# Kernel tuning notes

Measured on AMD Instinct MI355X. Metric: run time of the kernel, lower is better.

Reference implementation:

```python
import jax, jax.numpy as jnp
import numpy as np

N_NODES = 50000
N_EDGES = 400000
N_GRAPHS = 64
D_IN = 200
D_HID = 32
N_CLASS = 2


def setup_inputs() -> dict:
    key = jax.random.key(0)
    ks = jax.random.split(key, 16)
    x = jax.random.normal(ks[0], (N_NODES, D_IN), dtype=jnp.float32)
    edge_index = jax.random.randint(ks[1], (2, N_EDGES), 0, N_NODES, dtype=jnp.int64)
    edge_attr = jax.random.normal(ks[2], (N_EDGES,), dtype=jnp.float32)
    batch = jnp.sort(jax.random.randint(ks[3], (N_NODES,), 0, N_GRAPHS, dtype=jnp.int64))
    s = 0.05
    params = dict(
        W1r=jax.random.normal(ks[4], (D_IN, D_HID), jnp.float32) * s,
        W1l=jax.random.normal(ks[5], (D_IN, D_HID), jnp.float32) * s,
        b1=jnp.zeros((D_HID,), jnp.float32),
        W2r=jax.random.normal(ks[6], (D_HID, D_HID), jnp.float32) * s,
        W2l=jax.random.normal(ks[7], (D_HID, D_HID), jnp.float32) * s,
        b2=jnp.zeros((D_HID,), jnp.float32),
        W3r=jax.random.normal(ks[8], (D_HID, D_HID), jnp.float32) * s,
        W3l=jax.random.normal(ks[9], (D_HID, D_HID), jnp.float32) * s,
        b3=jnp.zeros((D_HID,), jnp.float32),
        Wlin=jax.random.normal(ks[10], (D_HID, N_CLASS), jnp.float32) * s,
        blin=jnp.zeros((N_CLASS,), jnp.float32),
    )
    return dict(x=x, edge_index=edge_index, edge_attr=edge_attr, batch=batch, **params)


def _graph_conv(x, src, dst, Wr, Wl, b):
    # PyG GraphConv: out_i = lin_rel(sum_{j->i} x_j) + lin_root(x_i)
    agg = jax.ops.segment_sum(x[src], dst, num_segments=x.shape[0])  # [N, d_in]
    return agg @ Wr + b + x @ Wl


def reference(x, edge_index, edge_attr, batch,
              W1r, W1l, b1, W2r, W2l, b2, W3r, W3l, b3, Wlin, blin):
    src, dst = edge_index[0], edge_index[1]
    # dropout is identity at inference (training=False)
    h = jax.nn.elu(_graph_conv(x, src, dst, W1r, W1l, b1))
    h = jax.nn.elu(_graph_conv(h, src, dst, W2r, W2l, b2))
    h = jax.nn.elu(_graph_conv(h, src, dst, W3r, W3l, b3))
    # global mean pool over graphs
    sums = jax.ops.segment_sum(h, batch, num_segments=N_GRAPHS)  # [G, d]
    counts = jax.ops.segment_sum(jnp.ones((h.shape[0],), h.dtype), batch,
                                 num_segments=N_GRAPHS)
    pooled = sums / jnp.maximum(counts, 1.0)[:, None]
    logits = pooled @ Wlin + blin
    return jax.nn.log_softmax(logits, axis=1)
```

## Files before the change

### kernel.cpp

```cpp
#include <hip/hip_runtime.h>
#include <hip/hip_bf16.h>


#define D_IN 200
#define N_GRAPHS 64

#define KP 232
#define KB 7
#define WT_ELEMS (64 * KP)
#define W23_ELEMS 2048

#define NT 256
#define NSCB 196
#define HS_STR 40

typedef __attribute__((ext_vector_type(8))) short bf16x8;
typedef __attribute__((ext_vector_type(4))) float f32x4;

__device__ __forceinline__ float4 elu4(float4 v) {
    float4 o;
    o.x = (v.x > 0.f) ? v.x : expm1f(v.x);
    o.y = (v.y > 0.f) ? v.y : expm1f(v.y);
    o.z = (v.z > 0.f) ? v.z : expm1f(v.z);
    o.w = (v.w > 0.f) ? v.w : expm1f(v.w);
    return o;
}

__global__ __launch_bounds__(NT) void count_pack(const int* __restrict__ dst,
                                                 int* __restrict__ cnt,
                                                 int* __restrict__ rank, int E,
                                                 const float* __restrict__ W1r,
                                                 const float* __restrict__ W1l,
                                                 const float* __restrict__ W2r,
                                                 const float* __restrict__ W2l,
                                                 const float* __restrict__ W3r,
                                                 const float* __restrict__ W3l,
                                                 __hip_bfloat16* __restrict__ Wt,
                                                 __hip_bfloat16* __restrict__ Wt2,
                                                 __hip_bfloat16* __restrict__ Wt3,
                                                 int egrid, int wgrid) {
    int blk = blockIdx.x;
    if (blk < egrid) {
        int e = blk * NT + threadIdx.x;
        if (e < E) rank[e] = atomicAdd(&cnt[dst[e]], 1);
    } else if (blk < egrid + wgrid) {
        int idx = (blk - egrid) * NT + threadIdx.x;
        if (idx < WT_ELEMS) {
            int n = idx / KP, k = idx % KP;
            float v = 0.f;
            if (k < D_IN) v = (n < 32) ? W1r[k * 32 + n] : W1l[k * 32 + (n - 32)];
            Wt[idx] = __float2bfloat16(v);
        }
    } else {
        int idx = (blk - egrid - wgrid) * NT + threadIdx.x;
        if (idx < 2 * W23_ELEMS) {
            int which = idx >> 11;
            int j = idx & 2047;
            int n = j >> 5, k = j & 31;
            const float* Wr = which ? W3r : W2r;
            const float* Wl = which ? W3l : W2l;
            float v = (n < 32) ? Wr[k * 32 + n] : Wl[k * 32 + (n - 32)];
            (which ? Wt3 : Wt2)[j] = __float2bfloat16(v);
        }
    }
}

__global__ __launch_bounds__(NT) void scan_fused(const int* __restrict__ cnt,
                                                 int* __restrict__ row_ptr,
                                                 int* __restrict__ partialSum,
                                                 int* __restrict__ flag, int N) {
    __shared__ int s[NT];
    int tile = blockIdx.x, tid = threadIdx.x;
    int idx = tile * NT + tid;
    int v = (idx < N) ? cnt[idx] : 0;
    s[tid] = v;
    __syncthreads();
    for (int off = 1; off < NT; off <<= 1) {
        int u = (tid >= off) ? s[tid - off] : 0;
        __syncthreads();
        s[tid] += u;
        __syncthreads();
    }
    int excl = s[tid] - v;
    int total = s[NT - 1];
    if (tid == 0) {
        __hip_atomic_store(&partialSum[tile], total, __ATOMIC_RELAXED, __HIP_MEMORY_SCOPE_AGENT);
        __hip_atomic_store(&flag[tile], 1, __ATOMIC_RELEASE, __HIP_MEMORY_SCOPE_AGENT);
    }
    int ps = 0;
    if (tid < tile) {
        while (__hip_atomic_load(&flag[tid], __ATOMIC_ACQUIRE, __HIP_MEMORY_SCOPE_AGENT) == 0) {}
        ps = __hip_atomic_load(&partialSum[tid], __ATOMIC_RELAXED, __HIP_MEMORY_SCOPE_AGENT);
    }
    __syncthreads();
    s[tid] = ps;
    __syncthreads();
    for (int off = 128; off > 0; off >>= 1) {
        if (tid < off) s[tid] += s[tid + off];
        __syncthreads();
    }
    int rp = s[0] + excl;
    if (idx < N) row_ptr[idx] = rp;
    if (idx == N - 1) row_ptr[N] = rp + v;
}

__global__ __launch_bounds__(NT) void fill_gemm1(const int* __restrict__ src,
                                                 const int* __restrict__ dst,
                                                 const int* __restrict__ rank,
                                                 const int* __restrict__ row_ptr,
                                                 int* __restrict__ colIdx, int E,
                                                 const float* __restrict__ X,
                                                 const __hip_bfloat16* __restrict__ Wt,
                                                 __hip_bfloat16* __restrict__ yr16,
                                                 float* __restrict__ yl, int N) {
    int tid = threadIdx.x, bid = blockIdx.x, nb = gridDim.x;
    for (int e = bid * NT + tid; e < E; e += nb * NT) {
        int d = dst[e];
        colIdx[row_ptr[d] + rank[e]] = src[e];
    }
    int lane = tid & 63, wv = tid >> 6;
    int l15 = lane & 15, q = lane >> 4;
    int ntile = (N + 63) >> 6;
    for (int tile = bid; tile < ntile; tile += nb) {
        long base = (long)tile * 64;
        long row = base + wv * 16 + l15;
        long rowc = (row < (long)N) ? row : (long)(N - 1);
        const float* xr = X + rowc * D_IN;
        bf16x8 a[KB];
#pragma unroll
        for (int kb = 0; kb < KB; ++kb) {
            int k0 = kb * 32 + q * 8;
            union { __hip_bfloat16 h[8]; bf16x8 v; } u;
            if (k0 + 8 <= D_IN) {
                float4 v0 = *(const float4*)(xr + k0);
                float4 v1 = *(const float4*)(xr + k0 + 4);
                u.h[0] = __float2bfloat16(v0.x); u.h[1] = __float2bfloat16(v0.y);
                u.h[2] = __float2bfloat16(v0.z); u.h[3] = __float2bfloat16(v0.w);
                u.h[4] = __float2bfloat16(v1.x); u.h[5] = __float2bfloat16(v1.y);
                u.h[6] = __float2bfloat16(v1.z); u.h[7] = __float2bfloat16(v1.w);
            } else {
#pragma unroll
                for (int j = 0; j < 8; ++j) {
                    int k = k0 + j;
                    u.h[j] = __float2bfloat16(k < D_IN ? xr[k] : 0.f);
                }
            }
            a[kb] = u.v;
        }
#pragma unroll
        for (int ns = 0; ns < 4; ++ns) {
            f32x4 acc = {0.f, 0.f, 0.f, 0.f};
#pragma unroll
            for (int kb = 0; kb < KB; ++kb) {
                bf16x8 bfrag = *(const bf16x8*)(const void*)
                    (Wt + (ns * 16 + l15) * KP + kb * 32 + q * 8);
                acc = __builtin_amdgcn_mfma_f32_16x16x32_bf16(a[kb], bfrag, acc, 0, 0, 0);
            }
            int col = ns * 16 + l15;
#pragma unroll
            for (int r = 0; r < 4; ++r) {
                long node = base + wv * 16 + q * 4 + r;
                if (node < N) {
                    if (col < 32) yr16[node * 32 + col] = __float2bfloat16(acc[r]);
                    else          yl[node * 32 + (col - 32)] = acc[r];
                }
            }
        }
    }
}

__device__ __forceinline__ void agg_node(const __hip_bfloat16* __restrict__ yr16,
                                         const float* __restrict__ yl,
                                         const int* __restrict__ row_ptr,
                                         const int* __restrict__ colIdx,
                                         const float* __restrict__ b,
                                         int node, int ln, float4& oA, float4& oB) {
    const uint4* yv = (const uint4*)yr16;
    int s = row_ptr[node], e = row_ptr[node + 1];
    int f0 = ln * 8;
    float4 bA = *(const float4*)(b + f0);
    float4 bB = *(const float4*)(b + f0 + 4);
    float4 rA = *(const float4*)(yl + (long)node * 32 + f0);
    float4 rB = *(const float4*)(yl + (long)node * 32 + f0 + 4);
    float acc[8] = {0.f, 0.f, 0.f, 0.f, 0.f, 0.f, 0.f, 0.f};
    for (int p = s; p < e; p += 8) {
        int jj[8]; float m[8];
#pragma unroll
        for (int i = 0; i < 8; ++i) {
            int pi = p + i;
            m[i] = (pi < e) ? 1.f : 0.f;
            pi = (pi < e) ? pi : (e - 1);
            jj[i] = colIdx[pi];
        }
        uint4 v[8];
#pragma unroll
        for (int i = 0; i < 8; ++i) v[i] = yv[(long)jj[i] * 4 + ln];
#pragma unroll
        for (int i = 0; i < 8; ++i) {
            uint d0 = v[i].x, d1 = v[i].y, d2 = v[i].z, d3 = v[i].w;
            acc[0] = fmaf(__uint_as_float(d0 << 16),          m[i], acc[0]);
            acc[1] = fmaf(__uint_as_float(d0 & 0xffff0000u),  m[i], acc[1]);
            acc[2] = fmaf(__uint_as_float(d1 << 16),          m[i], acc[2]);
            acc[3] = fmaf(__uint_as_float(d1 & 0xffff0000u),  m[i], acc[3]);
            acc[4] = fmaf(__uint_as_float(d2 << 16),          m[i], acc[4]);
            acc[5] = fmaf(__uint_as_float(d2 & 0xffff0000u),  m[i], acc[5]);
            acc[6] = fmaf(__uint_as_float(d3 << 16),          m[i], acc[6]);
            acc[7] = fmaf(__uint_as_float(d3 & 0xffff0000u),  m[i], acc[7]);
        }
    }
    oA = elu4(make_float4(acc[0] + bA.x + rA.x, acc[1] + bA.y + rA.y,
                          acc[2] + bA.z + rA.z, acc[3] + bA.w + rA.w));
    oB = elu4(make_float4(acc[4] + bB.x + rB.x, acc[5] + bB.y + rB.y,
                          acc[6] + bB.z + rB.z, acc[7] + bB.w + rB.w));
}

__global__ __launch_bounds__(NT) void agg_gemm_mfma(
        const __hip_bfloat16* __restrict__ yr16_in, const float* __restrict__ yl_in,
        const int* __restrict__ row_ptr, const int* __restrict__ colIdx,
        const float* __restrict__ b, const __hip_bfloat16* __restrict__ Wt2,
        __hip_bfloat16* __restrict__ yr16_out, float* __restrict__ yl_out, int N) {
    __shared__ __hip_bfloat16 hs[64 * HS_STR];
    int tid = threadIdx.x;
    int ln = tid & 3;
    int nl = tid >> 2;
    long base = (long)blockIdx.x * 64;
    int node = (int)base + nl;
    union { __hip_bfloat16 h[8]; float4 v; } u;
    if (node < N) {
        float4 oA, oB;
        agg_node(yr16_in, yl_in, row_ptr, colIdx, b, node, ln, oA, oB);
        u.h[0] = __float2bfloat16(oA.x); u.h[1] = __float2bfloat16(oA.y);
        u.h[2] = __float2bfloat16(oA.z); u.h[3] = __float2bfloat16(oA.w);
        u.h[4] = __float2bfloat16(oB.x); u.h[5] = __float2bfloat16(oB.y);
        u.h[6] = __float2bfloat16(oB.z); u.h[7] = __float2bfloat16(oB.w);
    } else {
        u.v = make_float4(0.f, 0.f, 0.f, 0.f);
    }
    *(float4*)(&hs[nl * HS_STR + ln * 8]) = u.v;
    __syncthreads();

    int lane = tid & 63, wv = tid >> 6;
    int l15 = lane & 15, q = lane >> 4;
    bf16x8 a = *(const bf16x8*)(const void*)(&hs[(wv * 16 + l15) * HS_STR + q * 8]);
#pragma unroll
    for (int ns = 0; ns < 4; ++ns) {
        f32x4 acc = {0.f, 0.f, 0.f, 0.f};
        bf16x8 bfrag = *(const bf16x8*)(const void*)(Wt2 + (ns * 16 + l15) * 32 + q * 8);
        acc = __builtin_amdgcn_mfma_f32_16x16x32_bf16(a, bfrag, acc, 0, 0, 0);
        int col = ns * 16 + l15;
#pragma unroll
        for (int r = 0; r < 4; ++r) {
            long nd = base + wv * 16 + q * 4 + r;
            if (nd < N) {
                if (col < 32) yr16_out[nd * 32 + col] = __float2bfloat16(acc[r]);
                else          yl_out[nd * 32 + (col - 32)] = acc[r];
            }
        }
    }
}

__global__ __launch_bounds__(NT) void agg_elu_k(const __hip_bfloat16* __restrict__ yr16,
                                                const float* __restrict__ yl,
                                                const int* __restrict__ row_ptr,
                                                const int* __restrict__ colIdx,
                                                const float* __restrict__ b,
                                                float* __restrict__ hout, int N) {
    int tid = threadIdx.x;
    int ln = tid & 3;
    int node = blockIdx.x * 64 + (tid >> 2);
    if (node >= N) return;
    float4 oA, oB;
    agg_node(yr16, yl, row_ptr, colIdx, b, node, ln, oA, oB);
    int f0 = ln * 8;
    *(float4*)(hout + (long)node * 32 + f0) = oA;
    *(float4*)(hout + (long)node * 32 + f0 + 4) = oB;
}

__global__ __launch_bounds__(NT) void pool_head(const float4* __restrict__ h4,
                                                const int* __restrict__ batch,
                                                const float* __restrict__ Wlin,
                                                const float* __restrict__ blin,
                                                float* __restrict__ out, int N) {
    int g = blockIdx.x;
    int lo = 0, hi = N;
    while (lo < hi) { int mid = (lo + hi) >> 1; if (batch[mid] < g) lo = mid + 1; else hi = mid; }
    int start = lo;
    hi = N;
    while (lo < hi) { int mid = (lo + hi) >> 1; if (batch[mid] < g + 1) lo = mid + 1; else hi = mid; }
    int end = lo;

    int f4 = threadIdx.x & 7, r = threadIdx.x >> 3;
    float4 acc = make_float4(0.f, 0.f, 0.f, 0.f);
    for (int i = start + r; i < end; i += 32) {
        float4 v = h4[(long)i * 8 + f4];
        acc.x += v.x; acc.y += v.y; acc.z += v.z; acc.w += v.w;
    }
    __shared__ float4 red[32][8];
    __shared__ float pooledS[32];
    red[r][f4] = acc;
    __syncthreads();
    if (r == 0) {
        float4 s = make_float4(0.f, 0.f, 0.f, 0.f);
#pragma unroll
        for (int r2 = 0; r2 < 32; ++r2) {
            float4 v = red[r2][f4];
            s.x += v.x; s.y += v.y; s.z += v.z; s.w += v.w;
        }
        float inv = 1.f / fmaxf((float)(end - start), 1.f);
        pooledS[f4 * 4 + 0] = s.x * inv;
        pooledS[f4 * 4 + 1] = s.y * inv;
        pooledS[f4 * 4 + 2] = s.z * inv;
        pooledS[f4 * 4 + 3] = s.w * inv;
    }
    __syncthreads();
    if (threadIdx.x == 0) {
        float c0 = blin[0], c1 = blin[1];
        for (int k = 0; k < 32; ++k) {
            float pk = pooledS[k];
            c0 += pk * Wlin[k * 2 + 0];
            c1 += pk * Wlin[k * 2 + 1];
        }
        float m = fmaxf(c0, c1);
        float lse = m + logf(expf(c0 - m) + expf(c1 - m));
        out[g * 2 + 0] = c0 - lse;
        out[g * 2 + 1] = c1 - lse;
    }
}

extern "C" void kernel_launch(void* const* d_in, const int* in_sizes, int n_in,
                              void* d_out, int out_size, void* d_ws, size_t ws_size,
                              hipStream_t stream) {
    const float* x     = (const float*)d_in[0];
    const int*   eidx  = (const int*)d_in[1];
    const int*   batch = (const int*)d_in[3];
    const float* W1r = (const float*)d_in[4];
    const float* W1l = (const float*)d_in[5];
    const float* b1  = (const float*)d_in[6];
    const float* W2r = (const float*)d_in[7];
    const float* W2l = (const float*)d_in[8];
    const float* b2  = (const float*)d_in[9];
    const float* W3r = (const float*)d_in[10];
    const float* W3l = (const float*)d_in[11];
    const float* b3  = (const float*)d_in[12];
    const float* Wlin = (const float*)d_in[13];
    const float* blin = (const float*)d_in[14];
    float* out = (float*)d_out;

    const int N = in_sizes[0] / D_IN;
    const int E = in_sizes[1] / 2;
    const int* src = eidx;
    const int* dst = eidx + E;

    char* w = (char*)d_ws;
    auto alloc = [&](size_t bytes) -> void* {
        void* p = (void*)w;
        w += (bytes + 255) & ~(size_t)255;
        return p;
    };
    int* cnt     = (int*)alloc((size_t)N * 4);
    int* flag    = (int*)alloc((size_t)256 * 4);
    int* rank    = (int*)alloc((size_t)E * 4);
    int* row_ptr = (int*)alloc((size_t)(N + 1) * 4);
    int* colIdx  = (int*)alloc((size_t)E * 4);
    int* partial = (int*)alloc((size_t)256 * 4);
    __hip_bfloat16* Wt    = (__hip_bfloat16*)alloc((size_t)WT_ELEMS * 2);
    __hip_bfloat16* Wt2   = (__hip_bfloat16*)alloc((size_t)W23_ELEMS * 2);
    __hip_bfloat16* Wt3   = (__hip_bfloat16*)alloc((size_t)W23_ELEMS * 2);
    __hip_bfloat16* yr16A = (__hip_bfloat16*)alloc((size_t)N * 32 * 2);
    __hip_bfloat16* yr16B = (__hip_bfloat16*)alloc((size_t)N * 32 * 2);
    float* ylA = (float*)alloc((size_t)N * 32 * 4);
    float* ylB = (float*)alloc((size_t)N * 32 * 4);
    float* hA  = (float*)alloc((size_t)N * 32 * 4);

    hipMemsetAsync(cnt, 0, (((size_t)N * 4 + 255) & ~(size_t)255) + 1024, stream);

    int egrid = (E + NT - 1) / NT;
    int wgrid = (WT_ELEMS + NT - 1) / NT;
    int w23g  = (2 * W23_ELEMS + NT - 1) / NT;
    int t64   = (N + 63) / 64;

    count_pack<<<egrid + wgrid + w23g, NT, 0, stream>>>(
        dst, cnt, rank, E, W1r, W1l, W2r, W2l, W3r, W3l, Wt, Wt2, Wt3, egrid, wgrid);
    scan_fused<<<NSCB, NT, 0, stream>>>(cnt, row_ptr, partial, flag, N);
    fill_gemm1<<<t64, NT, 0, stream>>>(src, dst, rank, row_ptr, colIdx, E, x, Wt, yr16A, ylA, N);
    agg_gemm_mfma<<<t64, NT, 0, stream>>>(yr16A, ylA, row_ptr, colIdx, b1, Wt2,
                                          yr16B, ylB, N);
    agg_gemm_mfma<<<t64, NT, 0, stream>>>(yr16B, ylB, row_ptr, colIdx, b2, Wt3,
                                          yr16A, ylA, N);
    agg_elu_k<<<t64, NT, 0, stream>>>(yr16A, ylA, row_ptr, colIdx, b3, hA, N);
    pool_head<<<N_GRAPHS, NT, 0, stream>>>((const float4*)hA, batch, Wlin, blin, out, N);
}
```

Measured before the change: 199.4 us.

## Fuse final aggregation with mean-pool and classifier head via atomics and last-block

Merges the third-layer aggregation+ELU kernel with the pooling/head kernel. Each block stages its 64 node outputs in shared memory, does a run-length segmented sum by graph id, and atomically adds into a small pooled buffer. The last block, found with an atomic counter, computes the means, linear head and log-softmax. This removes the 6.4MB h write/read and one kernel launch, at the cost of global float atomics and a serialized tail in the last block.

```diff
diff --git a/kernel.cpp b/kernel.cpp
--- a/kernel.cpp
+++ b/kernel.cpp
@@ -259,64 +259,65 @@
     }
 }
 
-__global__ __launch_bounds__(NT) void agg_elu_k(const __hip_bfloat16* __restrict__ yr16,
-                                                const float* __restrict__ yl,
-                                                const int* __restrict__ row_ptr,
-                                                const int* __restrict__ colIdx,
-                                                const float* __restrict__ b,
-                                                float* __restrict__ hout, int N) {
+__global__ __launch_bounds__(NT) void agg3_poolhead(
+        const __hip_bfloat16* __restrict__ yr16_in, const float* __restrict__ yl_in,
+        const int* __restrict__ row_ptr, const int* __restrict__ colIdx,
+        const float* __restrict__ b, const int* __restrict__ batch,
+        const float* __restrict__ Wlin, const float* __restrict__ blin,
+        float* __restrict__ out, float* __restrict__ pooled,
+        int* __restrict__ done, int N) {
+    __shared__ __align__(16) float hsf[64][32];
+    __shared__ int gids[64];
+    __shared__ int lastS;
     int tid = threadIdx.x;
     int ln = tid & 3;
-    int node = blockIdx.x * 64 + (tid >> 2);
-    if (node >= N) return;
-    float4 oA, oB;
-    agg_node(yr16, yl, row_ptr, colIdx, b, node, ln, oA, oB);
-    int f0 = ln * 8;
-    *(float4*)(hout + (long)node * 32 + f0) = oA;
-    *(float4*)(hout + (long)node * 32 + f0 + 4) = oB;
-}
-
-__global__ __launch_bounds__(NT) void pool_head(const float4* __restrict__ h4,
-                                                const int* __restrict__ batch,
-                                                const float* __restrict__ Wlin,
-                                                const float* __restrict__ blin,
-                                                float* __restrict__ out, int N) {
-    int g = blockIdx.x;
-    int lo = 0, hi = N;
-    while (lo < hi) { int mid = (lo + hi) >> 1; if (batch[mid] < g) lo = mid + 1; else hi = mid; }
-    int start = lo;
-    hi = N;
-    while (lo < hi) { int mid = (lo + hi) >> 1; if (batch[mid] < g + 1) lo = mid + 1; else hi = mid; }
-    int end = lo;
-
-    int f4 = threadIdx.x & 7, r = threadIdx.x >> 3;
-    float4 acc = make_float4(0.f, 0.f, 0.f, 0.f);
-    for (int i = start + r; i < end; i += 32) {
-        float4 v = h4[(long)i * 8 + f4];
-        acc.x += v.x; acc.y += v.y; acc.z += v.z; acc.w += v.w;
-    }
-    __shared__ float4 red[32][8];
-    __shared__ float pooledS[32];
-    red[r][f4] = acc;
-    __syncthreads();
-    if (r == 0) {
-        float4 s = make_float4(0.f, 0.f, 0.f, 0.f);
-#pragma unroll
-        for (int r2 = 0; r2 < 32; ++r2) {
-            float4 v = red[r2][f4];
-            s.x += v.x; s.y += v.y; s.z += v.z; s.w += v.w;
-        }
+    int nl = tid >> 2;
+    int node = blockIdx.x * 64 + nl;
+    bool valid = node < N;
+    float4 oA = make_float4(0.f, 0.f, 0.f, 0.f), oB = oA;
+    if (valid) agg_node(yr16_in, yl_in, row_ptr, colIdx, b, node, ln, oA, oB);
+    *(float4*)(&hsf[nl][ln * 8]) = oA;
+    *(float4*)(&hsf[nl][ln * 8 + 4]) = oB;
+    if (ln == 0) gids[nl] = valid ? batch[node] : -1;
+    __syncthreads();
+
+    if (tid < 64) {
+        int f = tid & 31, half = tid >> 5;
+        int i0 = half * 32, i1 = i0 + 32;
+        float acc = 0.f;
+        int gcur = gids[i0];
+        for (int i = i0; i < i1; ++i) {
+            int g = gids[i];
+            if (g != gcur) {
+                if (gcur >= 0) atomicAdd(&pooled[gcur * 32 + f], acc);
+                acc = 0.f; gcur = g;
+            }
+            acc += hsf[i][f];
+        }
+        if (gcur >= 0) atomicAdd(&pooled[gcur * 32 + f], acc);
+    }
+    __syncthreads();
+
+    if (tid == 0) {
+        int old = __hip_atomic_fetch_add(done, 1, __ATOMIC_ACQ_REL, __HIP_MEMORY_SCOPE_AGENT);
+        lastS = (old == (int)gridDim.x - 1) ? 1 : 0;
+    }
+    __syncthreads();
+    if (!lastS) return;
+
+    if (tid < N_GRAPHS) {
+        int g = tid;
+        int lo = 0, hi = N;
+        while (lo < hi) { int mid = (lo + hi) >> 1; if (batch[mid] < g) lo = mid + 1; else hi = mid; }
+        int start = lo;
+        hi = N;
+        while (lo < hi) { int mid = (lo + hi) >> 1; if (batch[mid] < g + 1) lo = mid + 1; else hi = mid; }
+        int end = lo;
         float inv = 1.f / fmaxf((float)(end - start), 1.f);
-        pooledS[f4 * 4 + 0] = s.x * inv;
-        pooledS[f4 * 4 + 1] = s.y * inv;
-        pooledS[f4 * 4 + 2] = s.z * inv;
-        pooledS[f4 * 4 + 3] = s.w * inv;
-    }
-    __syncthreads();
-    if (threadIdx.x == 0) {
         float c0 = blin[0], c1 = blin[1];
         for (int k = 0; k < 32; ++k) {
-            float pk = pooledS[k];
+            float pk = __hip_atomic_load(&pooled[g * 32 + k], __ATOMIC_RELAXED,
+                                         __HIP_MEMORY_SCOPE_AGENT) * inv;
             c0 += pk * Wlin[k * 2 + 0];
             c1 += pk * Wlin[k * 2 + 1];
         }
@@ -357,8 +358,12 @@
         w += (bytes + 255) & ~(size_t)255;
         return p;
     };
-    int* cnt     = (int*)alloc((size_t)N * 4);
-    int* flag    = (int*)alloc((size_t)256 * 4);
+    char* zbase = w;
+    int*   cnt    = (int*)alloc((size_t)N * 4);
+    int*   flag   = (int*)alloc((size_t)256 * 4);
+    float* pooled = (float*)alloc((size_t)N_GRAPHS * 32 * 4);
+    int*   done   = (int*)alloc((size_t)256 * 4);
+    size_t zbytes = (size_t)(w - zbase);
     int* rank    = (int*)alloc((size_t)E * 4);
     int* row_ptr = (int*)alloc((size_t)(N + 1) * 4);
     int* colIdx  = (int*)alloc((size_t)E * 4);
@@ -370,9 +375,8 @@
     __hip_bfloat16* yr16B = (__hip_bfloat16*)alloc((size_t)N * 32 * 2);
     float* ylA = (float*)alloc((size_t)N * 32 * 4);
     float* ylB = (float*)alloc((size_t)N * 32 * 4);
-    float* hA  = (float*)alloc((size_t)N * 32 * 4);
-
-    hipMemsetAsync(cnt, 0, (((size_t)N * 4 + 255) & ~(size_t)255) + 1024, stream);
+
+    hipMemsetAsync(zbase, 0, zbytes, stream);
 
     int egrid = (E + NT - 1) / NT;
     int wgrid = (WT_ELEMS + NT - 1) / NT;
@@ -387,6 +391,6 @@
                                           yr16B, ylB, N);
     agg_gemm_mfma<<<t64, NT, 0, stream>>>(yr16B, ylB, row_ptr, colIdx, b2, Wt3,
                                           yr16A, ylA, N);
-    agg_elu_k<<<t64, NT, 0, stream>>>(yr16A, ylA, row_ptr, colIdx, b3, hA, N);
-    pool_head<<<N_GRAPHS, NT, 0, stream>>>((const float4*)hA, batch, Wlin, blin, out, N);
-}
+    agg3_poolhead<<<t64, NT, 0, stream>>>(yr16A, ylA, row_ptr, colIdx, b3, batch,
+                                          Wlin, blin, out, pooled, done, N);
+}
```

Measured after the change: 204.2 us. 1.02x slower.
